# Optimization experiments

Measured on AMD Instinct MI355X. Metric: run time of the kernel, lower is better.

The kernel has to match this reference:

```python
import jax, jax.numpy as jnp
import numpy as np

N = 200000      # active sites
C = 128         # channels (inplanes == planes)
H = W = 1024    # spatial grid for coordinate hashing
K = 9           # 3x3 kernel offsets


def _build_nbr_idx(rng):
    """Rulebook for a 3x3 submanifold conv: nbr_idx[n, k] = row index of the
    active neighbor of site n at kernel offset k, or N (sentinel) if that
    neighbor is inactive or out of grid."""
    lin = rng.choice(H * W, size=N, replace=False).astype(np.int64)
    lookup = np.full(H * W, N, dtype=np.int32)
    lookup[lin] = np.arange(N, dtype=np.int32)
    y, x = lin // W, lin % W
    nbr = np.full((N, K), N, dtype=np.int32)
    k = 0
    for dy in (-1, 0, 1):
        for dx in (-1, 0, 1):
            ny, nx = y + dy, x + dx
            valid = (ny >= 0) & (ny < H) & (nx >= 0) & (nx < W)
            nl = np.where(valid, ny * W + nx, 0)
            nbr[:, k] = np.where(valid, lookup[nl], N)
            k += 1
    return nbr


def setup_inputs() -> dict:
    key = jax.random.key(0)
    k1, k2, k3 = jax.random.split(key, 3)
    rng = np.random.default_rng(0)
    scale = 1.0 / np.sqrt(K * C)
    return {
        "feats": jax.random.normal(k1, (N, C), dtype=jnp.float32),
        "nbr_idx": jnp.asarray(_build_nbr_idx(rng)),
        "W1": jax.random.normal(k2, (K, C, C), dtype=jnp.float32) * scale,
        "W2": jax.random.normal(k3, (K, C, C), dtype=jnp.float32) * scale,
    }


def _subm_conv(f, Wk, nbr_idx):
    # gather-GEMM: pad with a zero row so sentinel index N reads zeros
    fp = jnp.concatenate([f, jnp.zeros((1, f.shape[1]), f.dtype)], axis=0)
    g = fp[nbr_idx]                       # [N, K, Cin]
    return jnp.einsum('nkc,kco->no', g, Wk)  # [N, Cout]


def reference(feats, nbr_idx, W1, W2):
    # out = relu(conv2(relu(conv1(x))) + x), both convs 3x3 submanifold, no bias
    out = jax.nn.relu(_subm_conv(feats, W1, nbr_idx))
    out = _subm_conv(out, W2, nbr_idx)
    return jax.nn.relu(out + feats)
```

## Files before the change

### kernel.cpp

```cpp
#include <hip/hip_runtime.h>

#define CD 128
#define KK 9

typedef __bf16 bf16x8 __attribute__((ext_vector_type(8)));
typedef float  f32x4  __attribute__((ext_vector_type(4)));
typedef float  f32x16 __attribute__((ext_vector_type(16)));

typedef __attribute__((address_space(1))) const void* gas_ptr;
typedef __attribute__((address_space(3))) void*       las_ptr;

#define CAST_BLOCKS 2030
__global__ __launch_bounds__(256) void prep_kernel(
    const float* __restrict__ feats, unsigned short* __restrict__ fb16,
    const float* __restrict__ W1, const float* __restrict__ W2,
    unsigned short* __restrict__ W1T, unsigned short* __restrict__ W2T,
    const long total8) {
    if (blockIdx.x < 2 * KK) {
        __shared__ unsigned short tile[128 * 129];
        const int b = blockIdx.x;
        const int k = (b < KK) ? b : b - KK;
        const float* src = ((b < KK) ? W1 : W2) + k * (CD * CD);
        unsigned short* dst = ((b < KK) ? W1T : W2T) + k * (CD * CD);
        #pragma unroll 4
        for (int p = 0; p < 64; ++p) {
            int idx = p * 256 + threadIdx.x;
            int c = idx >> 7, o = idx & 127;
            __bf16 h = (__bf16)src[idx];
            tile[o * 129 + c] = __builtin_bit_cast(unsigned short, h);
        }
        __syncthreads();
        #pragma unroll 4
        for (int p = 0; p < 64; ++p) {
            int idx = p * 256 + threadIdx.x;
            int o = idx >> 7, c = idx & 127;
            dst[idx] = tile[o * 129 + c];
        }
    } else {
        const long stride = (long)CAST_BLOCKS * 256;
        for (long i = (long)(blockIdx.x - 2 * KK) * 256 + threadIdx.x;
             i < total8; i += stride) {
            f32x4 lo = *(const f32x4*)(feats + i * 8);
            f32x4 hi = *(const f32x4*)(feats + i * 8 + 4);
            bf16x8 v;
            #pragma unroll
            for (int e = 0; e < 4; ++e) {
                v[e]     = (__bf16)lo[e];
                v[e + 4] = (__bf16)hi[e];
            }
            *(bf16x8*)(fb16 + i * 8) = v;
        }
    }
}

template <bool FIRST>
__device__ __forceinline__ void conv_body(
    const unsigned short* __restrict__ asrc,
    const float* __restrict__ resid,
    const unsigned short* __restrict__ WT,
    const int* __restrict__ nbr,
    unsigned short* __restrict__ hout,
    float* __restrict__ fout,
    const int n, char (*wbuf)[32768])
{
    const int tid  = threadIdx.x;
    const int lane = tid & 63;
    const int l31  = lane & 31;
    const int kh   = lane >> 5;
    const int wave = tid >> 6;
    const int base = blockIdx.x * 256 + wave * 64;
    const int s0 = base + l31;
    const int s1 = base + 32 + l31;
    const int sc0 = (s0 < n) ? s0 : (n - 1);
    const int sc1 = (s1 < n) ? s1 : (n - 1);

    auto stage = [&](int b, int k) {
        const char* tap = (const char*)(WT + (size_t)k * CD * CD);
        char* lb = &wbuf[b][0];
        #pragma unroll
        for (int i = 0; i < 8; ++i) {
            const int chunk = (i * 4 + wave) * 1024;
            const int d = chunk + lane * 16;
            const int s = d ^ (((d >> 8) & 7) << 4);
            __builtin_amdgcn_global_load_lds((gas_ptr)(tap + s),
                                             (las_ptr)(lb + chunk), 16, 0, 0);
        }
    };

    f32x16 acc[2][4];
    if (FIRST) {
        #pragma unroll
        for (int m = 0; m < 2; ++m)
            #pragma unroll
            for (int nf = 0; nf < 4; ++nf)
                #pragma unroll
                for (int i = 0; i < 16; ++i) acc[m][nf][i] = 0.f;
    }

    int c0 = nbr[(size_t)sc0 * KK];
    int c1 = nbr[(size_t)sc1 * KK];
    stage(0, 0);

    if (!FIRST) {
        #pragma unroll
        for (int m = 0; m < 2; ++m)
            #pragma unroll
            for (int rg = 0; rg < 16; ++rg) {
                const int row  = (rg & 3) + 8 * (rg >> 2) + 4 * kh;
                const int srow = base + m * 32 + row;
                #pragma unroll
                for (int nf = 0; nf < 4; ++nf) {
                    float r = 0.f;
                    if (srow < n)
                        r = __builtin_nontemporal_load(
                                resid + (size_t)srow * CD + nf * 32 + l31);
                    acc[m][nf][rg] = r;
                }
            }
    }
    __syncthreads();

    bf16x8 zed;
    #pragma unroll
    for (int e = 0; e < 8; ++e) zed[e] = (__bf16)0.f;

    const int swq = (l31 & 7) << 4;

    #pragma unroll 1
    for (int k = 0; k < KK; ++k) {
        const bool v0 = (unsigned)c0 < (unsigned)n;
        const bool v1 = (unsigned)c1 < (unsigned)n;
        const size_t rr0 = (size_t)(v0 ? c0 : 0) * CD;
        const size_t rr1 = (size_t)(v1 ? c1 : 0) * CD;

        bf16x8 a0[8], a1[8];
        #pragma unroll
        for (int cs = 0; cs < 8; ++cs) {
            const int coff = cs * 16 + kh * 8;
            a0[cs] = *(const bf16x8*)(asrc + rr0 + coff);
            a1[cs] = *(const bf16x8*)(asrc + rr1 + coff);
            a0[cs] = v0 ? a0[cs] : zed;
            a1[cs] = v1 ? a1[cs] : zed;
        }

        int n0 = 0, n1 = 0;
        if (k + 1 < KK) {
            n0 = nbr[(size_t)sc0 * KK + k + 1];
            n1 = nbr[(size_t)sc1 * KK + k + 1];
            stage((k + 1) & 1, k + 1);
        }

        const char* wb = &wbuf[k & 1][0];
        #pragma unroll
        for (int cs = 0; cs < 8; ++cs) {
            #pragma unroll
            for (int nf = 0; nf < 4; ++nf) {
                const int x = ((nf * 32 + l31) << 8) + (cs << 5) + (kh << 4);
                bf16x8 b = *(const bf16x8*)(wb + (x ^ swq));
                acc[0][nf] = __builtin_amdgcn_mfma_f32_32x32x16_bf16(a0[cs], b, acc[0][nf], 0, 0, 0);
                acc[1][nf] = __builtin_amdgcn_mfma_f32_32x32x16_bf16(a1[cs], b, acc[1][nf], 0, 0, 0);
            }
        }

        __syncthreads();
        c0 = n0; c1 = n1;
    }

    #pragma unroll
    for (int m = 0; m < 2; ++m) {
        #pragma unroll
        for (int rg = 0; rg < 16; ++rg) {
            const int row  = (rg & 3) + 8 * (rg >> 2) + 4 * kh;
            const int srow = base + m * 32 + row;
            if (srow < n) {
                #pragma unroll
                for (int nf = 0; nf < 4; ++nf) {
                    float v = acc[m][nf][rg];
                    v = v > 0.f ? v : 0.f;
                    const size_t oi = (size_t)srow * CD + nf * 32 + l31;
                    if (FIRST) {
                        hout[oi] = __builtin_bit_cast(unsigned short, (__bf16)v);
                    } else {
                        __builtin_nontemporal_store(v, fout + oi);
                    }
                }
            }
        }
    }
}

__global__ __launch_bounds__(256, 2) void conv1_kernel(
    const unsigned short* __restrict__ fb16,
    const unsigned short* __restrict__ WT,
    const int* __restrict__ nbr,
    unsigned short* __restrict__ hout,
    const int n)
{
    __shared__ __align__(16) char wbuf[2][32768];
    conv_body<true>(fb16, nullptr, WT, nbr, hout, nullptr, n, wbuf);
}

__global__ __launch_bounds__(256, 2) void conv2_kernel(
    const unsigned short* __restrict__ hid,
    const float* __restrict__ feats,
    const unsigned short* __restrict__ WT,
    const int* __restrict__ nbr,
    float* __restrict__ fout,
    const int n)
{
    __shared__ __align__(16) char wbuf[2][32768];
    conv_body<false>(hid, feats, WT, nbr, nullptr, fout, n, wbuf);
}

extern "C" void kernel_launch(void* const* d_in, const int* in_sizes, int n_in,
                              void* d_out, int out_size, void* d_ws, size_t ws_size,
                              hipStream_t stream) {
    const float* feats = (const float*)d_in[0];
    const int*   nbr   = (const int*)d_in[1];
    const float* W1    = (const float*)d_in[2];
    const float* W2    = (const float*)d_in[3];
    float* out = (float*)d_out;

    const int n = in_sizes[0] / CD;

    unsigned short* hid  = (unsigned short*)d_ws;
    unsigned short* W1T  = hid + (size_t)n * CD;
    unsigned short* W2T  = W1T + KK * CD * CD;
    unsigned short* fb16 = W2T + KK * CD * CD;
    const size_t need = ((size_t)n * CD * 2 + (size_t)2 * KK * CD * CD) * 2;
    if (ws_size < need) {
        fb16 = (unsigned short*)d_out;
    }

    const long total8 = (long)n * CD / 8;
    prep_kernel<<<2 * KK + CAST_BLOCKS, 256, 0, stream>>>(
        feats, fb16, W1, W2, W1T, W2T, total8);

    const int grid = (n + 255) / 256;
    conv1_kernel<<<grid, 256, 0, stream>>>(fb16, W1T, nbr, hid, n);
    conv2_kernel<<<grid, 256, 0, stream>>>(hid, feats, W2T, nbr, out, n);
}
```

Before: 225.3 us.

## Software-pipeline neighbor feature gathers one tap ahead with double-buffered registers

Restructures the tap loop so the gathered A-operand rows for tap k+1 are loaded into a second register set while the MFMAs for tap k run, and neighbor indices are fetched two taps ahead. The loop is unrolled by two to ping-pong between register buffers. The intent is to hide gather latency behind matrix work, at the cost of doubling A-fragment register usage, which could cause spills or lower occupancy. Nontemporal load and store hints on the residual and output are also replaced with plain accesses.

```diff
diff --git a/kernel.cpp b/kernel.cpp
--- a/kernel.cpp
+++ b/kernel.cpp
@@ -88,6 +88,29 @@
     };
 
     f32x16 acc[2][4];
+
+    bf16x8 aA0[8], aA1[8], aB0[8], aB1[8];
+    bool vA0, vA1, vB0, vB1;
+    int i1_0, i1_1;
+
+    {
+        const int c0 = nbr[(size_t)sc0 * KK];
+        const int c1 = nbr[(size_t)sc1 * KK];
+        vA0 = (unsigned)c0 < (unsigned)n;
+        vA1 = (unsigned)c1 < (unsigned)n;
+        const size_t rr0 = (size_t)(vA0 ? c0 : 0) * CD;
+        const size_t rr1 = (size_t)(vA1 ? c1 : 0) * CD;
+        #pragma unroll
+        for (int cs = 0; cs < 8; ++cs) {
+            const int coff = cs * 16 + kh * 8;
+            aA0[cs] = *(const bf16x8*)(asrc + rr0 + coff);
+            aA1[cs] = *(const bf16x8*)(asrc + rr1 + coff);
+        }
+    }
+    stage(0, 0);
+    i1_0 = nbr[(size_t)sc0 * KK + 1];
+    i1_1 = nbr[(size_t)sc1 * KK + 1];
+
     if (FIRST) {
         #pragma unroll
         for (int m = 0; m < 2; ++m)
@@ -95,13 +118,7 @@
             for (int nf = 0; nf < 4; ++nf)
                 #pragma unroll
                 for (int i = 0; i < 16; ++i) acc[m][nf][i] = 0.f;
-    }
-
-    int c0 = nbr[(size_t)sc0 * KK];
-    int c1 = nbr[(size_t)sc1 * KK];
-    stage(0, 0);
-
-    if (!FIRST) {
+    } else {
         #pragma unroll
         for (int m = 0; m < 2; ++m)
             #pragma unroll
@@ -112,8 +129,7 @@
                 for (int nf = 0; nf < 4; ++nf) {
                     float r = 0.f;
                     if (srow < n)
-                        r = __builtin_nontemporal_load(
-                                resid + (size_t)srow * CD + nf * 32 + l31);
+                        r = resid[(size_t)srow * CD + nf * 32 + l31];
                     acc[m][nf][rg] = r;
                 }
             }
@@ -126,45 +142,59 @@
 
     const int swq = (l31 & 7) << 4;
 
-    #pragma unroll 1
-    for (int k = 0; k < KK; ++k) {
-        const bool v0 = (unsigned)c0 < (unsigned)n;
-        const bool v1 = (unsigned)c1 < (unsigned)n;
-        const size_t rr0 = (size_t)(v0 ? c0 : 0) * CD;
-        const size_t rr1 = (size_t)(v1 ? c1 : 0) * CD;
-
-        bf16x8 a0[8], a1[8];
+    auto do_tap = [&](int k, bf16x8 (&cur0)[8], bf16x8 (&cur1)[8],
+                      bool vc0, bool vc1,
+                      bf16x8 (&nxt0)[8], bf16x8 (&nxt1)[8]) {
+        if (k + 1 < KK) {
+            const size_t rn0 = (size_t)(((unsigned)i1_0 < (unsigned)n) ? i1_0 : 0) * CD;
+            const size_t rn1 = (size_t)(((unsigned)i1_1 < (unsigned)n) ? i1_1 : 0) * CD;
+            #pragma unroll
+            for (int cs = 0; cs < 8; ++cs) {
+                const int coff = cs * 16 + kh * 8;
+                nxt0[cs] = *(const bf16x8*)(asrc + rn0 + coff);
+                nxt1[cs] = *(const bf16x8*)(asrc + rn1 + coff);
+            }
+            stage((k + 1) & 1, k + 1);
+        }
+        const char* wb = &wbuf[k & 1][0];
         #pragma unroll
         for (int cs = 0; cs < 8; ++cs) {
-            const int coff = cs * 16 + kh * 8;
-            a0[cs] = *(const bf16x8*)(asrc + rr0 + coff);
-            a1[cs] = *(const bf16x8*)(asrc + rr1 + coff);
-            a0[cs] = v0 ? a0[cs] : zed;
-            a1[cs] = v1 ? a1[cs] : zed;
-        }
-
-        int n0 = 0, n1 = 0;
-        if (k + 1 < KK) {
-            n0 = nbr[(size_t)sc0 * KK + k + 1];
-            n1 = nbr[(size_t)sc1 * KK + k + 1];
-            stage((k + 1) & 1, k + 1);
-        }
-
-        const char* wb = &wbuf[k & 1][0];
-        #pragma unroll
-        for (int cs = 0; cs < 8; ++cs) {
+            const bf16x8 am0 = vc0 ? cur0[cs] : zed;
+            const bf16x8 am1 = vc1 ? cur1[cs] : zed;
             #pragma unroll
             for (int nf = 0; nf < 4; ++nf) {
                 const int x = ((nf * 32 + l31) << 8) + (cs << 5) + (kh << 4);
                 bf16x8 b = *(const bf16x8*)(wb + (x ^ swq));
-                acc[0][nf] = __builtin_amdgcn_mfma_f32_32x32x16_bf16(a0[cs], b, acc[0][nf], 0, 0, 0);
-                acc[1][nf] = __builtin_amdgcn_mfma_f32_32x32x16_bf16(a1[cs], b, acc[1][nf], 0, 0, 0);
-            }
-        }
-
+                acc[0][nf] = __builtin_amdgcn_mfma_f32_32x32x16_bf16(am0, b, acc[0][nf], 0, 0, 0);
+                acc[1][nf] = __builtin_amdgcn_mfma_f32_32x32x16_bf16(am1, b, acc[1][nf], 0, 0, 0);
+            }
+        }
         __syncthreads();
-        c0 = n0; c1 = n1;
-    }
+    };
+
+    #pragma unroll 1
+    for (int kk = 0; kk < 4; ++kk) {
+        const int k = kk * 2;
+        const bool nv0 = (unsigned)i1_0 < (unsigned)n;
+        const bool nv1 = (unsigned)i1_1 < (unsigned)n;
+        const int t2_0 = nbr[(size_t)sc0 * KK + k + 2];
+        const int t2_1 = nbr[(size_t)sc1 * KK + k + 2];
+        do_tap(k, aA0, aA1, vA0, vA1, aB0, aB1);
+        vB0 = nv0; vB1 = nv1;
+        i1_0 = t2_0; i1_1 = t2_1;
+
+        const bool mv0 = (unsigned)i1_0 < (unsigned)n;
+        const bool mv1 = (unsigned)i1_1 < (unsigned)n;
+        int t3_0 = 0, t3_1 = 0;
+        if (k + 3 < KK) {
+            t3_0 = nbr[(size_t)sc0 * KK + k + 3];
+            t3_1 = nbr[(size_t)sc1 * KK + k + 3];
+        }
+        do_tap(k + 1, aB0, aB1, vB0, vB1, aA0, aA1);
+        vA0 = mv0; vA1 = mv1;
+        i1_0 = t3_0; i1_1 = t3_1;
+    }
+    do_tap(8, aA0, aA1, vA0, vA1, aB0, aB1);
 
     #pragma unroll
     for (int m = 0; m < 2; ++m) {
@@ -181,7 +211,7 @@
                     if (FIRST) {
                         hout[oi] = __builtin_bit_cast(unsigned short, (__bf16)v);
                     } else {
-                        __builtin_nontemporal_store(v, fout + oi);
+                        fout[oi] = v;
                     }
                 }
             }
```

Result: slower. 257.4 us (+14.2%).
